# Kernel tuning notes

Hardware: AMD Instinct MI355X
Metric: run time of the kernel (lower is better)

## Reference

```python
import jax, jax.numpy as jnp
import numpy as np

# Scalar quantization params (QLinear __init__ args)
FEATURE_BITWIDTH = 8
WEIGHT_BITWIDTH = 8
INPUT_ZERO_POINT = -3
OUTPUT_ZERO_POINT = -5
INPUT_SCALE = 0.05
OUTPUT_SCALE = 0.1
QMIN = -(1 << (FEATURE_BITWIDTH - 1))   # -128
QMAX = (1 << (FEATURE_BITWIDTH - 1)) - 1  # 127

M, K, N = 8192, 4096, 4096


def float_to_fixed_point(x, bitwidth):
    """Represent x (0 < x < 1) as int_scale * 2^-frac_bits with int_scale
    in [2^(bitwidth-2), 2^(bitwidth-1)) (mantissa fits in signed `bitwidth` bits)."""
    frac_bits = (bitwidth - 1 - jnp.ceil(jnp.log2(x))).astype(jnp.int32)
    int_scale = jnp.round(x * jnp.exp2(frac_bits.astype(jnp.float32))).astype(jnp.int32)
    return int_scale, frac_bits


def setup_inputs() -> dict:
    key = jax.random.key(0)
    k1, k2, k3, k4 = jax.random.split(key, 4)
    qinput = jax.random.randint(k1, (M, K), -128, 128, dtype=jnp.int8)
    qweight = jax.random.randint(k2, (N, K), -128, 128, dtype=jnp.int8)
    qbias = jax.random.randint(k3, (N,), -(1 << 16), 1 << 16, dtype=jnp.int32)
    # per-output-channel weight scale; keeps folded scale in (0, 1)
    weight_scale = jax.random.uniform(k4, (N,), jnp.float32, 0.002, 0.02)
    return {"qinput": qinput, "qweight": qweight, "qbias": qbias,
            "weight_scale": weight_scale}


def reference(qinput, qweight, qbias, weight_scale):
    w32 = qweight.astype(jnp.int32)                      # [N, K]
    # Qbias' = qbias - sum_k(qweight) * Zin  (bias shift folding input zero point)
    shifted_qbias = qbias - w32.sum(axis=1) * INPUT_ZERO_POINT  # [N]
    # int32 GEMM: [M, K] @ [K, N] + bias
    acc = qinput.astype(jnp.int32) @ w32.T + shifted_qbias[None, :]  # [M, N]
    # fixed-point requantization: (acc * int_scale) >> frac_bits + Zout
    folded_scale = INPUT_SCALE * weight_scale / OUTPUT_SCALE         # [N], in (0,1)
    int_scale, frac_bits = float_to_fixed_point(folded_scale, FEATURE_BITWIDTH)
    # widen to int64 for the multiply so the (acc * int_scale) product cannot wrap
    prod = acc.astype(jnp.int64) * int_scale.astype(jnp.int64)[None, :]
    scaled = jnp.right_shift(prod, frac_bits.astype(jnp.int64)[None, :])  # arithmetic >>
    out = scaled + OUTPUT_ZERO_POINT
    return jnp.clip(out, QMIN, QMAX).astype(jnp.int8)
```

## Files before the change

kernel.cpp:

```cpp
#include <hip/hip_runtime.h>
#include <cstdint>
#include <cstddef>

#define M_DIM 8192
#define N_DIM 4096
#define K_DIM 4096

#define BM 128
#define BN 128
#define BK 128

#define BM2 256
#define BN2 256
#define BK2 128
#define NKT (K_DIM / BK2)

typedef int int32x4  __attribute__((ext_vector_type(4)));
typedef int int32x16 __attribute__((ext_vector_type(16)));


typedef __attribute__((address_space(1))) const void* gas_cptr;
typedef __attribute__((address_space(3))) void* las_ptr;

__device__ __forceinline__ void async_copy16(const void* g, void* l) {
    __builtin_amdgcn_global_load_lds((gas_cptr)g, (las_ptr)l, 16, 0, 0);
}

__device__ __forceinline__ int32x4 pack16(const int* p) {
    const int32x4* v = (const int32x4*)p;
    int32x4 w0 = v[0], w1 = v[1], w2 = v[2], w3 = v[3];
    int32x4 r;
    r.x = (w0.x & 0xFF) | ((w0.y & 0xFF) << 8) | ((w0.z & 0xFF) << 16) | (w0.w << 24);
    r.y = (w1.x & 0xFF) | ((w1.y & 0xFF) << 8) | ((w1.z & 0xFF) << 16) | (w1.w << 24);
    r.z = (w2.x & 0xFF) | ((w2.y & 0xFF) << 8) | ((w2.z & 0xFF) << 16) | (w2.w << 24);
    r.w = (w3.x & 0xFF) | ((w3.y & 0xFF) << 8) | ((w3.z & 0xFF) << 16) | (w3.w << 24);
    return r;
}

__global__ void ql_detect_kernel(const int* a, const int* b, int* ws) {
    int t = threadIdx.x;
    int fa = 0, fb = 0;
    for (int i = t; i < 4096; i += 64) {
        int va = a[i]; if (va > 127 || va < -128) fa = 1;
        int vb = b[i]; if (vb > 127 || vb < -128) fb = 1;
    }
    unsigned long long ba = __ballot(fa);
    unsigned long long bb = __ballot(fb);
    if (t == 0) { ws[0] = ba ? 1 : 0; ws[1] = bb ? 1 : 0; }
}

#define PACK_WBLK 4096
#define PACK_ABLK 8192
__global__ __launch_bounds__(256)
void ql_pack2_kernel(const void* wsrc, int* wdst, const void* asrc, int* adst,
                     const int* qbias, const float* wscale, int* ws) {
    __shared__ int red[4];
    const int fA = __builtin_amdgcn_readfirstlane(ws[0]);
    const int fW = __builtin_amdgcn_readfirstlane(ws[1]);
    const int bid = blockIdx.x;
    const int tid = threadIdx.x;
    if (bid < PACK_WBLK) {
        if (fW) return;
        const int n = bid;
        const int32x4* src = (const int32x4*)wsrc + (size_t)n * 1024;
        int* dst = wdst + (size_t)n * 1024;
        int s = 0;
#pragma unroll
        for (int k = 0; k < 4; ++k) {
            const int i = k * 256 + tid;
            int32x4 v = src[i];
            s += v.x + v.y + v.z + v.w;
            dst[i] = (v.x & 0xFF) | ((v.y & 0xFF) << 8) | ((v.z & 0xFF) << 16) | (v.w << 24);
        }
#pragma unroll
        for (int off = 32; off > 0; off >>= 1) s += __shfl_down(s, off, 64);
        if ((tid & 63) == 0) red[tid >> 6] = s;
        __syncthreads();
        if (tid == 0) {
            const int st = red[0] + red[1] + red[2] + red[3];
            ws[16 + n] = qbias[n] + 3 * st;
            float folded = (0.05f * wscale[n]) / 0.1f;
            int fbits = (int)(7.0f - ceilf(log2f(folded)));
            int isc = (int)rintf(folded * exp2f((float)fbits));
            ws[16 + N_DIM + n] = isc;
            ws[16 + 2 * N_DIM + n] = fbits;
        }
    } else {
        if (fA) return;
        const long base = (long)(bid - PACK_WBLK) * 1024;
        const int32x4* src = (const int32x4*)asrc + base;
        int* dst = adst + base;
#pragma unroll
        for (int k = 0; k < 4; ++k) {
            const int i = k * 256 + tid;
            int32x4 v = src[i];
            dst[i] = (v.x & 0xFF) | ((v.y & 0xFF) << 8) | ((v.z & 0xFF) << 16) | (v.w << 24);
        }
    }
}

__global__ void ql_prep8_kernel(const void* worig, const int* qbias,
                                const float* wscale, int* ws) {
    const int fb = __builtin_amdgcn_readfirstlane(ws[1]);
    if (!fb) return;

    const int lane = threadIdx.x & 63;
    const int wid  = threadIdx.x >> 6;
    const int n = blockIdx.x * 4 + wid;

    const int32x4* row = (const int32x4*)((const int8_t*)worig + (size_t)n * K_DIM);
    int s = 0;
    for (int c = lane; c < K_DIM / 16; c += 64) {
        int32x4 v = row[c];
#pragma unroll
        for (int j = 0; j < 4; ++j) {
            int w = (j == 0) ? v.x : (j == 1) ? v.y : (j == 2) ? v.z : v.w;
            s += (int)(int8_t)(w) + (int)(int8_t)(w >> 8)
               + (int)(int8_t)(w >> 16) + (w >> 24);
        }
    }
#pragma unroll
    for (int off = 32; off > 0; off >>= 1) s += __shfl_down(s, off, 64);

    if (lane == 0) {
        ws[16 + n] = qbias[n] + 3 * s;
        float folded = (0.05f * wscale[n]) / 0.1f;
        int fbits = (int)(7.0f - ceilf(log2f(folded)));
        int isc = (int)rintf(folded * exp2f((float)fbits));
        ws[16 + N_DIM + n] = isc;
        ws[16 + 2 * N_DIM + n] = fbits;
    }
}

__global__ void ql_prep_kernel(const void* wptr, const int* qbias,
                               const float* wscale, int* ws) {
    const int lane = threadIdx.x & 63;
    const int wid  = threadIdx.x >> 6;
    const int n = blockIdx.x * 4 + wid;
    const int b8 = __builtin_amdgcn_readfirstlane(ws[1]);

    int s = 0;
    if (b8) {
        const int32x4* row = (const int32x4*)((const int8_t*)wptr + (size_t)n * K_DIM);
        for (int c = lane; c < K_DIM / 16; c += 64) {
            int32x4 v = row[c];
#pragma unroll
            for (int j = 0; j < 4; ++j) {
                int w = (j == 0) ? v.x : (j == 1) ? v.y : (j == 2) ? v.z : v.w;
                s += (int)(int8_t)(w) + (int)(int8_t)(w >> 8)
                   + (int)(int8_t)(w >> 16) + (w >> 24);
            }
        }
    } else {
        const int32x4* row = (const int32x4*)((const int*)wptr + (size_t)n * K_DIM);
        for (int c = lane; c < K_DIM / 4; c += 64) {
            int32x4 v = row[c];
            s += v.x + v.y + v.z + v.w;
        }
    }
#pragma unroll
    for (int off = 32; off > 0; off >>= 1) s += __shfl_down(s, off, 64);

    if (lane == 0) {
        ws[16 + n] = qbias[n] + 3 * s;
        float folded = (0.05f * wscale[n]) / 0.1f;
        int fbits = (int)(7.0f - ceilf(log2f(folded)));
        int isc = (int)rintf(folded * exp2f((float)fbits));
        ws[16 + N_DIM + n] = isc;
        ws[16 + 2 * N_DIM + n] = fbits;
    }
}

__device__ __forceinline__ void ql_epilogue(int32x4 acc[4][4], const int* ws,
                                            int* out, int bm, int bn,
                                            int wm, int wn, int qm, int qh) {
    const int* qb  = ws + 16;
    const int* isc = ws + 16 + N_DIM;
    const int* fbt = ws + 16 + 2 * N_DIM;
#pragma unroll
    for (int j = 0; j < 4; ++j) {
        const int n_g = bn * BN + wn + j * 16 + qm;
        const int b0 = qb[n_g];
        const int s0 = isc[n_g];
        const int f0 = fbt[n_g];
#pragma unroll
        for (int i = 0; i < 4; ++i) {
            const int m_base = bm * BM + wm + i * 16 + qh * 4;
#pragma unroll
            for (int r = 0; r < 4; ++r) {
                int v = ((r == 0) ? acc[i][j].x : (r == 1) ? acc[i][j].y
                        : (r == 2) ? acc[i][j].z : acc[i][j].w) + b0;
                long long p = (long long)v * (long long)s0;
                int o = (int)(p >> f0) - 5;
                o = o < -128 ? -128 : (o > 127 ? 127 : o);
                out[(size_t)(m_base + r) * N_DIM + n_g] = o;
            }
        }
    }
}


#define TILE2(BUF, TT, VMC, DOST) do { \
    asm volatile("s_waitcnt vmcnt(" #VMC ")" ::: "memory"); \
    __builtin_amdgcn_s_barrier(); \
    _Pragma("unroll") for (int ml = 0; ml < 2; ++ml) \
    _Pragma("unroll") for (int kc = 0; kc < 4; ++kc) \
        afL[ml][kc] = LA[BUF][baseAe[kc] + ml * 256]; \
    _Pragma("unroll") for (int kc = 0; kc < 4; ++kc) \
        bf0[kc] = LB[BUF][baseBe[kc]]; \
    _Pragma("unroll") for (int kc = 0; kc < 4; ++kc) \
        bf1[kc] = LB[BUF][baseBe[kc] + 256]; \
    _Pragma("unroll") for (int ml = 0; ml < 2; ++ml) \
    _Pragma("unroll") for (int kc = 0; kc < 4; ++kc) \
        afH[ml][kc] = LA[BUF][baseAe[kc] + 512 + ml * 256]; \
    __builtin_amdgcn_s_setprio(1); \
    _Pragma("unroll") for (int kc = 0; kc < 4; ++kc) \
    _Pragma("unroll") for (int ml = 0; ml < 2; ++ml) \
        acc[ml][0] = __builtin_amdgcn_mfma_i32_32x32x32_i8(afL[ml][kc], bf0[kc], acc[ml][0], 0, 0, 0); \
    _Pragma("unroll") for (int kc = 0; kc < 4; ++kc) \
    _Pragma("unroll") for (int ml = 0; ml < 2; ++ml) \
        acc[ml][1] = __builtin_amdgcn_mfma_i32_32x32x32_i8(afL[ml][kc], bf1[kc], acc[ml][1], 0, 0, 0); \
    _Pragma("unroll") for (int kc = 0; kc < 4; ++kc) \
    _Pragma("unroll") for (int ml = 0; ml < 2; ++ml) \
        acc[2 + ml][0] = __builtin_amdgcn_mfma_i32_32x32x32_i8(afH[ml][kc], bf0[kc], acc[2 + ml][0], 0, 0, 0); \
    _Pragma("unroll") for (int kc = 0; kc < 4; ++kc) \
    _Pragma("unroll") for (int ml = 0; ml < 2; ++ml) \
        acc[2 + ml][1] = __builtin_amdgcn_mfma_i32_32x32x32_i8(afH[ml][kc], bf1[kc], acc[2 + ml][1], 0, 0, 0); \
    __builtin_amdgcn_s_setprio(0); \
    __builtin_amdgcn_s_barrier(); \
    if (DOST) { \
        _Pragma("unroll") for (int h2 = 0; h2 < 4; ++h2) { \
            async_copy16(gA + (size_t)((TT) + 2) * 128 + (size_t)h2 * 262144, \
                         &LA[BUF][h2 * 512 + t]); \
            async_copy16(gB + (size_t)((TT) + 2) * 128 + (size_t)h2 * 262144, \
                         &LB[BUF][h2 * 512 + t]); \
        } \
    } \
} while (0)

__global__ __launch_bounds__(512, 2)
void ql_gemm8_kernel(const void* a0, const int8_t* a8,
                     const void* b0, const int8_t* w8,
                     const int* ws, int* out) {
    __shared__ int32x4 LA[2][2048];
    __shared__ int32x4 LB[2][2048];

    const int fa = __builtin_amdgcn_readfirstlane(ws[0]);
    const int fb = __builtin_amdgcn_readfirstlane(ws[1]);
    const int8_t* aptr = fa ? (const int8_t*)a0 : a8;
    const int8_t* bptr = fb ? (const int8_t*)b0 : w8;

    const int t    = threadIdx.x;
    const int lane = t & 63;
    const int wid  = t >> 6;
    const int wr   = wid >> 2;
    const int wc   = wid & 3;
    const int l31  = lane & 31;
    const int hi   = lane >> 5;

    const int flat = blockIdx.y * gridDim.x + blockIdx.x;
    const int xcd  = flat & 7;
    const int lid  = flat >> 3;
    const int g    = lid >> 5;
    const int r    = lid & 31;
    const int bm   = xcd * 4 + g * 2 + (r & 1);
    const int bn   = r >> 1;

    const int arow0 = bm * BM2;
    const int brow0 = bn * BN2;

    const int fr = (lane & 7) ^ ((l31 >> 3) & 3);
    int baseAe[4], baseBe[4];
#pragma unroll
    for (int kc = 0; kc < 4; ++kc) {
        const int phys = (kc * 2 + hi) ^ fr;
        baseAe[kc] = (wr * 128 + l31) * 8 + phys;
        baseBe[kc] = (wc * 64  + l31) * 8 + phys;
    }

    const int colg = (t & 7) ^ ((t >> 3) & 7) ^ ((t >> 6) & 3);
    const int8_t* gA = aptr + (size_t)(arow0 + (t >> 3)) * K_DIM + colg * 16;
    const int8_t* gB = bptr + (size_t)(brow0 + (t >> 3)) * K_DIM + colg * 16;

    int32x16 acc[4][2] = {};
    int32x4 afL[2][4], afH[2][4], bf0[4], bf1[4];

#pragma unroll
    for (int h2 = 0; h2 < 4; ++h2) {
        async_copy16(gA + (size_t)h2 * 262144, &LA[0][h2 * 512 + t]);
        async_copy16(gB + (size_t)h2 * 262144, &LB[0][h2 * 512 + t]);
    }
#pragma unroll
    for (int h2 = 0; h2 < 4; ++h2) {
        async_copy16(gA + 128 + (size_t)h2 * 262144, &LA[1][h2 * 512 + t]);
        async_copy16(gB + 128 + (size_t)h2 * 262144, &LB[1][h2 * 512 + t]);
    }

#pragma unroll 1
    for (int T = 0; T < NKT - 2; T += 2) {
        TILE2(0, T, 8, true);
        TILE2(1, T + 1, 8, true);
    }
    TILE2(0, NKT - 2, 8, false);
    TILE2(1, NKT - 1, 0, false);

    const int* qb  = ws + 16;
    const int* isc = ws + 16 + N_DIM;
    const int* fbt = ws + 16 + 2 * N_DIM;
#pragma unroll
    for (int j = 0; j < 2; ++j) {
        const int n_g = bn * BN2 + wc * 64 + j * 32 + l31;
        const int b0r = qb[n_g];
        const int s0r = isc[n_g];
        const int f0r = fbt[n_g];
#pragma unroll
        for (int i = 0; i < 4; ++i) {
            const int m0 = bm * BM2 + wr * 128 + i * 32 + hi * 4;
#pragma unroll
            for (int reg = 0; reg < 16; ++reg) {
                const int row = (reg & 3) + 8 * (reg >> 2);
                int v = acc[i][j][reg] + b0r;
                long long p = (long long)v * (long long)s0r;
                int o = (int)(p >> f0r) - 5;
                o = o < -128 ? -128 : (o > 127 ? 127 : o);
                __builtin_nontemporal_store(o, &out[(size_t)(m0 + row) * N_DIM + n_g]);
            }
        }
    }
}

__global__ __launch_bounds__(256)
void ql_gemm_fb_kernel(const void* aptr, const void* bptr, const int* ws, int* out) {
    __shared__ int32x4 Als[BM * BK / 16];
    __shared__ int32x4 Bls[BN * BK / 16];

    const int a8 = __builtin_amdgcn_readfirstlane(ws[0]);
    const int b8 = __builtin_amdgcn_readfirstlane(ws[1]);

    const int t    = threadIdx.x;
    const int lane = t & 63;
    const int wid  = t >> 6;
    const int bn = blockIdx.x;
    const int bm = blockIdx.y;

    const int wm = (wid >> 1) * 64;
    const int wn = (wid & 1) * 64;
    const int qm = lane & 15;
    const int qh = lane >> 4;

    int32x4 acc[4][4] = {};

    for (int kt = 0; kt < K_DIM / BK; ++kt) {
        __syncthreads();
        const int k0 = kt * BK;
#pragma unroll
        for (int r = 0; r < 4; ++r) {
            const int c    = r * 256 + t;
            const int row  = c >> 3;
            const int colg = (c & 7) ^ (row & 7);
            const size_t offA = (size_t)(bm * BM + row) * K_DIM + k0 + colg * 16;
            const size_t offB = (size_t)(bn * BN + row) * K_DIM + k0 + colg * 16;
            if (a8) async_copy16((const int8_t*)aptr + offA, &Als[c]);
            else    Als[c] = pack16((const int*)aptr + offA);
            if (b8) async_copy16((const int8_t*)bptr + offB, &Bls[c]);
            else    Bls[c] = pack16((const int*)bptr + offB);
        }
        __syncthreads();

#pragma unroll
        for (int s = 0; s < 2; ++s) {
            const int colk = s * 4 + qh;
            int32x4 af[4], bf[4];
#pragma unroll
            for (int i = 0; i < 4; ++i) {
                const int ra = wm + i * 16 + qm;
                const int rb = wn + i * 16 + qm;
                af[i] = Als[ra * 8 + (colk ^ (ra & 7))];
                bf[i] = Bls[rb * 8 + (colk ^ (rb & 7))];
            }
#pragma unroll
            for (int i = 0; i < 4; ++i)
#pragma unroll
                for (int j = 0; j < 4; ++j)
                    acc[i][j] = __builtin_amdgcn_mfma_i32_16x16x64_i8(
                        af[i], bf[j], acc[i][j], 0, 0, 0);
        }
    }
    ql_epilogue(acc, ws, out, bm, bn, wm, wn, qm, qh);
}

extern "C" void kernel_launch(void* const* d_in, const int* in_sizes, int n_in,
                              void* d_out, int out_size, void* d_ws, size_t ws_size,
                              hipStream_t stream) {
    const void* qin    = d_in[0];
    const void* qwt    = d_in[1];
    const int* qbias   = (const int*)d_in[2];
    const float* wscal = (const float*)d_in[3];
    int* ws  = (int*)d_ws;
    int* out = (int*)d_out;

    hipLaunchKernelGGL(ql_detect_kernel, dim3(1), dim3(64), 0, stream,
                       (const int*)qin, (const int*)qwt, ws);

    const size_t need = 65536 + (size_t)M_DIM * K_DIM + (size_t)N_DIM * K_DIM;
    if (ws_size >= need) {
        int8_t* a8 = (int8_t*)d_ws + 65536;
        int8_t* w8 = a8 + (size_t)M_DIM * K_DIM;
        hipLaunchKernelGGL(ql_pack2_kernel, dim3(PACK_WBLK + PACK_ABLK), dim3(256),
                           0, stream, qwt, (int*)w8, qin, (int*)a8, qbias, wscal, ws);
        hipLaunchKernelGGL(ql_prep8_kernel, dim3(N_DIM / 4), dim3(256), 0, stream,
                           qwt, qbias, wscal, ws);
        hipLaunchKernelGGL(ql_gemm8_kernel, dim3(N_DIM / BN2, M_DIM / BM2), dim3(512),
                           0, stream, qin, a8, qwt, w8, ws, out);
    } else {
        hipLaunchKernelGGL(ql_prep_kernel, dim3(N_DIM / 4), dim3(256), 0, stream,
                           qwt, qbias, wscal, ws);
        hipLaunchKernelGGL(ql_gemm_fb_kernel, dim3(N_DIM / BN, M_DIM / BM), dim3(256), 0, stream,
                           qin, qwt, ws, out);
    }
}
```

Before: 412.9 us.

## Restructure int8 GEMM to 4 waves with 128x128 warp tiles and register prefetch

```diff
diff --git a/kernel.cpp b/kernel.cpp
--- a/kernel.cpp
+++ b/kernel.cpp
@@ -200,45 +200,35 @@
 }
 
 
-#define TILE2(BUF, TT, VMC, DOST) do { \
-    asm volatile("s_waitcnt vmcnt(" #VMC ")" ::: "memory"); \
-    __builtin_amdgcn_s_barrier(); \
-    _Pragma("unroll") for (int ml = 0; ml < 2; ++ml) \
-    _Pragma("unroll") for (int kc = 0; kc < 4; ++kc) \
-        afL[ml][kc] = LA[BUF][baseAe[kc] + ml * 256]; \
-    _Pragma("unroll") for (int kc = 0; kc < 4; ++kc) \
-        bf0[kc] = LB[BUF][baseBe[kc]]; \
-    _Pragma("unroll") for (int kc = 0; kc < 4; ++kc) \
-        bf1[kc] = LB[BUF][baseBe[kc] + 256]; \
-    _Pragma("unroll") for (int ml = 0; ml < 2; ++ml) \
-    _Pragma("unroll") for (int kc = 0; kc < 4; ++kc) \
-        afH[ml][kc] = LA[BUF][baseAe[kc] + 512 + ml * 256]; \
-    __builtin_amdgcn_s_setprio(1); \
-    _Pragma("unroll") for (int kc = 0; kc < 4; ++kc) \
-    _Pragma("unroll") for (int ml = 0; ml < 2; ++ml) \
-        acc[ml][0] = __builtin_amdgcn_mfma_i32_32x32x32_i8(afL[ml][kc], bf0[kc], acc[ml][0], 0, 0, 0); \
-    _Pragma("unroll") for (int kc = 0; kc < 4; ++kc) \
-    _Pragma("unroll") for (int ml = 0; ml < 2; ++ml) \
-        acc[ml][1] = __builtin_amdgcn_mfma_i32_32x32x32_i8(afL[ml][kc], bf1[kc], acc[ml][1], 0, 0, 0); \
-    _Pragma("unroll") for (int kc = 0; kc < 4; ++kc) \
-    _Pragma("unroll") for (int ml = 0; ml < 2; ++ml) \
-        acc[2 + ml][0] = __builtin_amdgcn_mfma_i32_32x32x32_i8(afH[ml][kc], bf0[kc], acc[2 + ml][0], 0, 0, 0); \
-    _Pragma("unroll") for (int kc = 0; kc < 4; ++kc) \
-    _Pragma("unroll") for (int ml = 0; ml < 2; ++ml) \
-        acc[2 + ml][1] = __builtin_amdgcn_mfma_i32_32x32x32_i8(afH[ml][kc], bf1[kc], acc[2 + ml][1], 0, 0, 0); \
-    __builtin_amdgcn_s_setprio(0); \
-    __builtin_amdgcn_s_barrier(); \
+#define TILE4(BUF, TT, DOST) do { \
+    _Pragma("unroll") for (int i = 0; i < 4; ++i) af[0][i] = LA[BUF][baseAe[0] + i * 256]; \
+    _Pragma("unroll") for (int j = 0; j < 4; ++j) bf[0][j] = LB[BUF][baseBe[0] + j * 256]; \
     if (DOST) { \
-        _Pragma("unroll") for (int h2 = 0; h2 < 4; ++h2) { \
-            async_copy16(gA + (size_t)((TT) + 2) * 128 + (size_t)h2 * 262144, \
-                         &LA[BUF][h2 * 512 + t]); \
-            async_copy16(gB + (size_t)((TT) + 2) * 128 + (size_t)h2 * 262144, \
-                         &LB[BUF][h2 * 512 + t]); \
+        _Pragma("unroll") for (int h = 0; h < 8; ++h) { \
+            async_copy16(gA + (size_t)((TT) + 1) * 128 + (size_t)h * 131072, \
+                         &LA[(BUF) ^ 1][h * 256 + t]); \
+            async_copy16(gB + (size_t)((TT) + 1) * 128 + (size_t)h * 131072, \
+                         &LB[(BUF) ^ 1][h * 256 + t]); \
         } \
     } \
+    _Pragma("unroll") for (int kc = 0; kc < 4; ++kc) { \
+        if (kc < 3) { \
+            _Pragma("unroll") for (int i = 0; i < 4; ++i) \
+                af[kc + 1][i] = LA[BUF][baseAe[kc + 1] + i * 256]; \
+            _Pragma("unroll") for (int j = 0; j < 4; ++j) \
+                bf[kc + 1][j] = LB[BUF][baseBe[kc + 1] + j * 256]; \
+        } \
+        __builtin_amdgcn_s_setprio(1); \
+        _Pragma("unroll") for (int i = 0; i < 4; ++i) \
+        _Pragma("unroll") for (int j = 0; j < 4; ++j) \
+            acc[i][j] = __builtin_amdgcn_mfma_i32_32x32x32_i8( \
+                af[kc][i], bf[kc][j], acc[i][j], 0, 0, 0); \
+        __builtin_amdgcn_s_setprio(0); \
+    } \
+    __syncthreads(); \
 } while (0)
 
-__global__ __launch_bounds__(512, 2)
+__global__ __launch_bounds__(256, 1)
 void ql_gemm8_kernel(const void* a0, const int8_t* a8,
                      const void* b0, const int8_t* w8,
                      const int* ws, int* out) {
@@ -253,8 +243,8 @@
     const int t    = threadIdx.x;
     const int lane = t & 63;
     const int wid  = t >> 6;
-    const int wr   = wid >> 2;
-    const int wc   = wid & 3;
+    const int wr   = wid >> 1;
+    const int wc   = wid & 1;
     const int l31  = lane & 31;
     const int hi   = lane >> 5;
 
@@ -275,41 +265,37 @@
     for (int kc = 0; kc < 4; ++kc) {
         const int phys = (kc * 2 + hi) ^ fr;
         baseAe[kc] = (wr * 128 + l31) * 8 + phys;
-        baseBe[kc] = (wc * 64  + l31) * 8 + phys;
+        baseBe[kc] = (wc * 128 + l31) * 8 + phys;
     }
 
     const int colg = (t & 7) ^ ((t >> 3) & 7) ^ ((t >> 6) & 3);
     const int8_t* gA = aptr + (size_t)(arow0 + (t >> 3)) * K_DIM + colg * 16;
     const int8_t* gB = bptr + (size_t)(brow0 + (t >> 3)) * K_DIM + colg * 16;
 
-    int32x16 acc[4][2] = {};
-    int32x4 afL[2][4], afH[2][4], bf0[4], bf1[4];
-
-#pragma unroll
-    for (int h2 = 0; h2 < 4; ++h2) {
-        async_copy16(gA + (size_t)h2 * 262144, &LA[0][h2 * 512 + t]);
-        async_copy16(gB + (size_t)h2 * 262144, &LB[0][h2 * 512 + t]);
-    }
-#pragma unroll
-    for (int h2 = 0; h2 < 4; ++h2) {
-        async_copy16(gA + 128 + (size_t)h2 * 262144, &LA[1][h2 * 512 + t]);
-        async_copy16(gB + 128 + (size_t)h2 * 262144, &LB[1][h2 * 512 + t]);
-    }
+    int32x16 acc[4][4] = {};
+    int32x4 af[4][4], bf[4][4];
+
+#pragma unroll
+    for (int h = 0; h < 8; ++h) {
+        async_copy16(gA + (size_t)h * 131072, &LA[0][h * 256 + t]);
+        async_copy16(gB + (size_t)h * 131072, &LB[0][h * 256 + t]);
+    }
+    __syncthreads();
 
 #pragma unroll 1
     for (int T = 0; T < NKT - 2; T += 2) {
-        TILE2(0, T, 8, true);
-        TILE2(1, T + 1, 8, true);
-    }
-    TILE2(0, NKT - 2, 8, false);
-    TILE2(1, NKT - 1, 0, false);
+        TILE4(0, T, true);
+        TILE4(1, T + 1, true);
+    }
+    TILE4(0, NKT - 2, true);
+    TILE4(1, NKT - 1, false);
 
     const int* qb  = ws + 16;
     const int* isc = ws + 16 + N_DIM;
     const int* fbt = ws + 16 + 2 * N_DIM;
 #pragma unroll
-    for (int j = 0; j < 2; ++j) {
-        const int n_g = bn * BN2 + wc * 64 + j * 32 + l31;
+    for (int j = 0; j < 4; ++j) {
+        const int n_g = bn * BN2 + wc * 128 + j * 32 + l31;
         const int b0r = qb[n_g];
         const int s0r = isc[n_g];
         const int f0r = fbt[n_g];
@@ -410,7 +396,7 @@
                            0, stream, qwt, (int*)w8, qin, (int*)a8, qbias, wscal, ws);
         hipLaunchKernelGGL(ql_prep8_kernel, dim3(N_DIM / 4), dim3(256), 0, stream,
                            qwt, qbias, wscal, ws);
-        hipLaunchKernelGGL(ql_gemm8_kernel, dim3(N_DIM / BN2, M_DIM / BM2), dim3(512),
+        hipLaunchKernelGGL(ql_gemm8_kernel, dim3(N_DIM / BN2, M_DIM / BM2), dim3(256),
                            0, stream, qin, a8, qwt, w8, ws, out);
     } else {
         hipLaunchKernelGGL(ql_prep_kernel, dim3(N_DIM / 4), dim3(256), 0, stream,
```

New measurement: 425.0 us. 1.03x slower.

## Interleave half-tile LDS refills between MFMA quadrants for finer-grained pipelining

Applied to the files above, without the earlier changes.

```diff
diff --git a/kernel.cpp b/kernel.cpp
--- a/kernel.cpp
+++ b/kernel.cpp
@@ -200,42 +200,58 @@
 }
 
 
-#define TILE2(BUF, TT, VMC, DOST) do { \
-    asm volatile("s_waitcnt vmcnt(" #VMC ")" ::: "memory"); \
-    __builtin_amdgcn_s_barrier(); \
+#define LOAD_AF(BUF, MH, DST) do { \
     _Pragma("unroll") for (int ml = 0; ml < 2; ++ml) \
     _Pragma("unroll") for (int kc = 0; kc < 4; ++kc) \
-        afL[ml][kc] = LA[BUF][baseAe[kc] + ml * 256]; \
+        DST[ml][kc] = LA[BUF][baseAe[kc] + (MH) * 512 + ml * 256]; \
+} while (0)
+
+#define LOAD_BF(BUF, NH, DST) do { \
     _Pragma("unroll") for (int kc = 0; kc < 4; ++kc) \
-        bf0[kc] = LB[BUF][baseBe[kc]]; \
-    _Pragma("unroll") for (int kc = 0; kc < 4; ++kc) \
-        bf1[kc] = LB[BUF][baseBe[kc] + 256]; \
-    _Pragma("unroll") for (int ml = 0; ml < 2; ++ml) \
-    _Pragma("unroll") for (int kc = 0; kc < 4; ++kc) \
-        afH[ml][kc] = LA[BUF][baseAe[kc] + 512 + ml * 256]; \
+        DST[kc] = LB[BUF][baseBe[kc] + (NH) * 256]; \
+} while (0)
+
+#define MFMA_QUAD(MH, NH, AF, BF) do { \
     __builtin_amdgcn_s_setprio(1); \
     _Pragma("unroll") for (int kc = 0; kc < 4; ++kc) \
     _Pragma("unroll") for (int ml = 0; ml < 2; ++ml) \
-        acc[ml][0] = __builtin_amdgcn_mfma_i32_32x32x32_i8(afL[ml][kc], bf0[kc], acc[ml][0], 0, 0, 0); \
-    _Pragma("unroll") for (int kc = 0; kc < 4; ++kc) \
-    _Pragma("unroll") for (int ml = 0; ml < 2; ++ml) \
-        acc[ml][1] = __builtin_amdgcn_mfma_i32_32x32x32_i8(afL[ml][kc], bf1[kc], acc[ml][1], 0, 0, 0); \
-    _Pragma("unroll") for (int kc = 0; kc < 4; ++kc) \
-    _Pragma("unroll") for (int ml = 0; ml < 2; ++ml) \
-        acc[2 + ml][0] = __builtin_amdgcn_mfma_i32_32x32x32_i8(afH[ml][kc], bf0[kc], acc[2 + ml][0], 0, 0, 0); \
-    _Pragma("unroll") for (int kc = 0; kc < 4; ++kc) \
-    _Pragma("unroll") for (int ml = 0; ml < 2; ++ml) \
-        acc[2 + ml][1] = __builtin_amdgcn_mfma_i32_32x32x32_i8(afH[ml][kc], bf1[kc], acc[2 + ml][1], 0, 0, 0); \
+        acc[(MH) * 2 + ml][NH] = __builtin_amdgcn_mfma_i32_32x32x32_i8( \
+            AF[ml][kc], BF[kc], acc[(MH) * 2 + ml][NH], 0, 0, 0); \
     __builtin_amdgcn_s_setprio(0); \
-    __builtin_amdgcn_s_barrier(); \
-    if (DOST) { \
-        _Pragma("unroll") for (int h2 = 0; h2 < 4; ++h2) { \
-            async_copy16(gA + (size_t)((TT) + 2) * 128 + (size_t)h2 * 262144, \
-                         &LA[BUF][h2 * 512 + t]); \
-            async_copy16(gB + (size_t)((TT) + 2) * 128 + (size_t)h2 * 262144, \
-                         &LB[BUF][h2 * 512 + t]); \
-        } \
-    } \
+} while (0)
+
+#define STAGE_A(BUF, H, TT) do { \
+    async_copy16(gA + (size_t)(TT) * 128 + (H) * 524288,          &LA[BUF][(H) * 1024 + t]); \
+    async_copy16(gA + (size_t)(TT) * 128 + (H) * 524288 + 262144, &LA[BUF][(H) * 1024 + 512 + t]); \
+} while (0)
+
+#define STAGE_B(BUF, H, TT) do { \
+    async_copy16(gB + (size_t)(TT) * 128 + (H) * 524288,          &LB[BUF][(H) * 1024 + t]); \
+    async_copy16(gB + (size_t)(TT) * 128 + (H) * 524288 + 262144, &LB[BUF][(H) * 1024 + 512 + t]); \
+} while (0)
+
+#define TILE_BODY(BUF, TT, VMC) do { \
+    asm volatile("s_waitcnt vmcnt(" #VMC ")" ::: "memory"); \
+    __builtin_amdgcn_s_barrier(); \
+    LOAD_AF(BUF, 0, afL); \
+    LOAD_BF(BUF, 0, bf0); \
+    if ((TT) + 1 < NKT) { STAGE_A(BUF ^ 1, 1, (TT) + 1); } \
+    __builtin_amdgcn_s_barrier(); \
+    MFMA_QUAD(0, 0, afL, bf0); \
+    __builtin_amdgcn_s_barrier(); \
+    LOAD_BF(BUF, 1, bf1); \
+    if ((TT) + 1 < NKT) { STAGE_B(BUF ^ 1, 1, (TT) + 1); } \
+    __builtin_amdgcn_s_barrier(); \
+    MFMA_QUAD(0, 1, afL, bf1); \
+    __builtin_amdgcn_s_barrier(); \
+    LOAD_AF(BUF, 1, afH); \
+    if ((TT) + 2 < NKT) { STAGE_B(BUF, 0, (TT) + 2); } \
+    __builtin_amdgcn_s_barrier(); \
+    MFMA_QUAD(1, 0, afH, bf0); \
+    __builtin_amdgcn_s_barrier(); \
+    if ((TT) + 2 < NKT) { STAGE_A(BUF, 0, (TT) + 2); } \
+    __builtin_amdgcn_s_barrier(); \
+    MFMA_QUAD(1, 1, afH, bf1); \
 } while (0)
 
 __global__ __launch_bounds__(512, 2)
@@ -285,24 +301,17 @@
     int32x16 acc[4][2] = {};
     int32x4 afL[2][4], afH[2][4], bf0[4], bf1[4];
 
-#pragma unroll
-    for (int h2 = 0; h2 < 4; ++h2) {
-        async_copy16(gA + (size_t)h2 * 262144, &LA[0][h2 * 512 + t]);
-        async_copy16(gB + (size_t)h2 * 262144, &LB[0][h2 * 512 + t]);
-    }
-#pragma unroll
-    for (int h2 = 0; h2 < 4; ++h2) {
-        async_copy16(gA + 128 + (size_t)h2 * 262144, &LA[1][h2 * 512 + t]);
-        async_copy16(gB + 128 + (size_t)h2 * 262144, &LB[1][h2 * 512 + t]);
-    }
+    STAGE_A(0, 0, 0); STAGE_B(0, 0, 0);
+    STAGE_A(0, 1, 0); STAGE_B(0, 1, 0);
+    STAGE_B(1, 0, 1); STAGE_A(1, 0, 1);
 
 #pragma unroll 1
     for (int T = 0; T < NKT - 2; T += 2) {
-        TILE2(0, T, 8, true);
-        TILE2(1, T + 1, 8, true);
-    }
-    TILE2(0, NKT - 2, 8, false);
-    TILE2(1, NKT - 1, 0, false);
+        TILE_BODY(0, T, 4);
+        TILE_BODY(1, T + 1, 4);
+    }
+    TILE_BODY(0, NKT - 2, 4);
+    TILE_BODY(1, NKT - 1, 0);
 
     const int* qb  = ws + 16;
     const int* isc = ws + 16 + N_DIM;
```

New measurement: 416.0 us. About the same (+0.7%).
